# Performance work log

Hardware: AMD Instinct MI355X
Metric: run time of the kernel (lower is better)

The kernel has to match this reference:

```python
import jax, jax.numpy as jnp
import numpy as np

DIM, K, H, D, G = 1024, 4, 8, 128, 4

def rotate_half(x):
    x1, x2 = jnp.split(x, 2, axis=-1)
    return jnp.concatenate([-x2, x1], axis=-1)

def setup_inputs() -> dict:
    key = jax.random.key(0)
    ks = jax.random.split(key, 14)
    s = 0.02
    return {
        "x":  jax.random.normal(ks[0], (1, 2048, DIM), jnp.float32),
        "Wq": jax.random.normal(ks[1], (H * D, DIM), jnp.float32) * s,
        "bq": jnp.zeros((H * D,), jnp.float32),
        "Wk": jax.random.normal(ks[2], (G * D, DIM), jnp.float32) * s,
        "bk": jnp.zeros((G * D,), jnp.float32),
        "Wv": jax.random.normal(ks[3], (G * D, DIM), jnp.float32) * s,
        "bv": jnp.zeros((G * D,), jnp.float32),
        "Wo": jax.random.normal(ks[4], (DIM, H * D), jnp.float32) * s,
        "bo": jnp.zeros((DIM,), jnp.float32),
        "W1": jax.random.normal(ks[5], (DIM * 4, DIM), jnp.float32) * s,
        "b1": jnp.zeros((DIM * 4,), jnp.float32),
        "W2": jax.random.normal(ks[6], (K * DIM, DIM * 4), jnp.float32) * s,
        "b2": jnp.zeros((K * DIM,), jnp.float32),
    }

def reference(x, Wq, bq, Wk, bk, Wv, bv, Wo, bo, W1, b1, W2, b2):
    B, S, _ = x.shape
    q = (x @ Wq.T + bq).reshape(B, S, H, D).transpose(0, 2, 1, 3)  # (B,H,S,D)
    k = (x @ Wk.T + bk).reshape(B, S, G, D).transpose(0, 2, 1, 3)  # (B,G,S,D)
    v = (x @ Wv.T + bv).reshape(B, S, G, D).transpose(0, 2, 1, 3)
    # rotary embedding (same as RotaryEmbedding module)
    inv_freq = 1.0 / (10000.0 ** (jnp.arange(0, D, 2, dtype=jnp.float32) / D))
    t = jnp.arange(S, dtype=jnp.float32)
    freqs = t[:, None] * inv_freq[None, :]
    emb = jnp.concatenate([freqs, freqs], axis=-1)            # (S, D)
    cos = jnp.cos(emb)[None, None, :, :]
    sin = jnp.sin(emb)[None, None, :, :]
    q = q * cos + rotate_half(q) * sin
    k = k * cos + rotate_half(k) * sin
    # every q head attends to every kv group; softmax over j, then sum over g and j
    scores = jnp.einsum('bhid,bgjd->bhgij', q, k) / jnp.sqrt(jnp.float32(D))
    mask = jnp.triu(jnp.ones((S, S), dtype=bool), 1)
    scores = jnp.where(mask[None, None, None, :, :], -jnp.inf, scores)
    w = jax.nn.softmax(scores, axis=-1)
    attn = jnp.einsum('bhgij,bgjd->bhid', w, v)               # (B,H,S,D)
    attn = attn.transpose(0, 2, 1, 3).reshape(B, S, H * D)
    o = attn @ Wo.T + bo
    h1 = jax.nn.silu(o @ W1.T + b1)
    out = (h1 @ W2.T + b2).reshape(B, S, K, DIM)
    return out
```

## Files before the change

kernel.cpp:

```cpp
#include <hip/hip_runtime.h>
#include <hip/hip_bf16.h>

#define SEQ 2048

typedef unsigned short ushort_t;
typedef __attribute__((ext_vector_type(8))) short short8;
typedef __attribute__((ext_vector_type(4))) float f32x4;

__device__ __forceinline__ ushort_t f2bf(float f) {
    __hip_bfloat16 h = __float2bfloat16(f);
    return *reinterpret_cast<ushort_t*>(&h);
}

__device__ __forceinline__ void st(float* p, float v) { *p = v; }
__device__ __forceinline__ void st(ushort_t* p, float v) { *p = f2bf(v); }

__device__ __forceinline__ void gload16(const ushort_t* g, ushort_t* l) {
    __builtin_amdgcn_global_load_lds(
        (const __attribute__((address_space(1))) unsigned int*)g,
        (__attribute__((address_space(3))) unsigned int*)l, 16, 0, 0);
}

__global__ void cvt_bf_kernel(const float* __restrict__ s0, ushort_t* __restrict__ d0, int n0,
                              const float* __restrict__ s1, ushort_t* __restrict__ d1, int n1,
                              const float* __restrict__ s2, ushort_t* __restrict__ d2, int n2,
                              const float* __restrict__ s3, ushort_t* __restrict__ d3, int n3,
                              const float* __restrict__ s4, ushort_t* __restrict__ d4) {
    int u = blockIdx.x * 256 + threadIdx.x;
    const float* s; ushort_t* d;
    if (u < n0) { s = s0; d = d0; }
    else if ((u -= n0) < n1) { s = s1; d = d1; }
    else if ((u -= n1) < n2) { s = s2; d = d2; }
    else if ((u -= n2) < n3) { s = s3; d = d3; }
    else { u -= n3; s = s4; d = d4; }
    float4 a = ((const float4*)s)[u];
    union { ushort_t us[4]; unsigned long long ll; } pk;
    pk.us[0] = f2bf(a.x); pk.us[1] = f2bf(a.y);
    pk.us[2] = f2bf(a.z); pk.us[3] = f2bf(a.w);
    ((unsigned long long*)d)[u] = pk.ll;
}

template <bool SILU, typename TC>
__global__ __launch_bounds__(256) void mfma_gemm_kernel(
    const ushort_t* __restrict__ A, const ushort_t* __restrict__ W,
    const float* __restrict__ bias, TC* __restrict__ C, int M, int N, int Kd) {
    __shared__ __align__(16) ushort_t As[128 * 64];
    __shared__ __align__(16) ushort_t Bs[128 * 64];
    const int tid = threadIdx.x;
    const int w = tid >> 6, lane = tid & 63, l15 = lane & 15, quad = lane >> 4;
    const int m0 = blockIdx.y * 128, n0 = blockIdx.x * 128;
    const int rw = (w >> 1) * 64, cw = (w & 1) * 64;
    const int rA = w * 32 + (lane >> 3);
    const int cch = ((lane & 7) ^ (lane >> 3)) * 8;

    f32x4 acc[4][4];
#pragma unroll
    for (int mt = 0; mt < 4; ++mt)
#pragma unroll
        for (int nt = 0; nt < 4; ++nt) acc[mt][nt] = (f32x4){0.f, 0.f, 0.f, 0.f};

    for (int k0 = 0; k0 < Kd; k0 += 64) {
#pragma unroll
        for (int c = 0; c < 4; ++c) {
            gload16(&A[(size_t)(m0 + rA + c * 8) * Kd + k0 + cch],
                    &As[(w * 4 + c) * 512]);
            gload16(&W[(size_t)(n0 + rA + c * 8) * Kd + k0 + cch],
                    &Bs[(w * 4 + c) * 512]);
        }
        __syncthreads();
#pragma unroll
        for (int kc = 0; kc < 2; ++kc) {
            short8 af[4], bfr[4];
#pragma unroll
            for (int mt = 0; mt < 4; ++mt) {
                int row = rw + mt * 16 + l15;
                int slot = (kc * 4 + quad) ^ (row & 7);
                af[mt] = *(const short8*)&As[row * 64 + slot * 8];
            }
#pragma unroll
            for (int nt = 0; nt < 4; ++nt) {
                int row = cw + nt * 16 + l15;
                int slot = (kc * 4 + quad) ^ (row & 7);
                bfr[nt] = *(const short8*)&Bs[row * 64 + slot * 8];
            }
#pragma unroll
            for (int mt = 0; mt < 4; ++mt)
#pragma unroll
                for (int nt = 0; nt < 4; ++nt)
                    acc[mt][nt] = __builtin_amdgcn_mfma_f32_16x16x32_bf16(
                        af[mt], bfr[nt], acc[mt][nt], 0, 0, 0);
        }
        __syncthreads();
    }
#pragma unroll
    for (int nt = 0; nt < 4; ++nt) {
        int col = n0 + cw + nt * 16 + l15;
        float bb = bias[col];
#pragma unroll
        for (int mt = 0; mt < 4; ++mt)
#pragma unroll
            for (int r = 0; r < 4; ++r) {
                int row = m0 + rw + mt * 16 + quad * 4 + r;
                float v = acc[mt][nt][r] + bb;
                if (SILU) v = v / (1.f + __expf(-v));
                st(&C[(size_t)row * N + col], v);
            }
    }
}

__global__ void rope_bf_kernel(const float* __restrict__ qf, const float* __restrict__ kf,
                               ushort_t* __restrict__ qb, ushort_t* __restrict__ kb) {
    const int s = blockIdx.x;
    const float t = (float)s;
    const float qs = 0.08838834764831845f;
    for (int p = threadIdx.x; p < 768; p += 256) {
        int idx = p & 63;
        float invf = powf(10000.f, -(float)(2 * idx) / 128.f);
        float ang = t * invf;
        float c = cosf(ang), sn = sinf(ang);
        if (p < 512) {
            int h = p >> 6;
            const float* src = qf + (size_t)s * 1024 + h * 128 + idx;
            ushort_t* dst = qb + (size_t)s * 1024 + h * 128 + idx;
            float x1 = src[0], x2 = src[64];
            dst[0] = f2bf((x1 * c - x2 * sn) * qs);
            dst[64] = f2bf((x2 * c + x1 * sn) * qs);
        } else {
            int h = (p - 512) >> 6;
            const float* src = kf + (size_t)s * 512 + h * 128 + idx;
            ushort_t* dst = kb + (size_t)s * 512 + h * 128 + idx;
            float x1 = src[0], x2 = src[64];
            dst[0] = f2bf(x1 * c - x2 * sn);
            dst[64] = f2bf(x2 * c + x1 * sn);
        }
    }
}

__global__ void transpose_v_kernel(const ushort_t* __restrict__ v, ushort_t* __restrict__ vT) {
    __shared__ __align__(16) ushort_t t[64][72];
    const int s0 = blockIdx.x * 64, d0 = blockIdx.y * 64;
    const int tid = threadIdx.x;
#pragma unroll
    for (int it = 0; it < 2; ++it) {
        int u = tid + it * 256;
        int r = u >> 3, c8 = u & 7;
        *(short8*)&t[r][c8 * 8] = *(const short8*)&v[(size_t)(s0 + r) * 512 + d0 + c8 * 8];
    }
    __syncthreads();
#pragma unroll
    for (int it = 0; it < 2; ++it) {
        int u = tid + it * 256;
        int r = u >> 3, c8 = u & 7;
        short8 o;
        ushort_t* op = (ushort_t*)&o;
#pragma unroll
        for (int i = 0; i < 8; ++i) op[i] = t[c8 * 8 + i][r];
        *(short8*)&vT[(size_t)(d0 + r) * 2048 + s0 + c8 * 8] = o;
    }
}

__global__ __launch_bounds__(256, 2) void mfma_attn_kernel(
    const ushort_t* __restrict__ qb, const ushort_t* __restrict__ kb,
    const ushort_t* __restrict__ vT, float* __restrict__ part) {
    const int tid = threadIdx.x;
    const int w = tid >> 6;
    const int lane = tid & 63;
    const int l15 = lane & 15;
    const int quad = lane >> 4;
    const int bx = blockIdx.x;
    const int pr = bx >> 3;
    const int g = (bx >> 1) & 3;
    const int h = (bx & 1) * 4 + w;

    const ushort_t* vtg = vT + (size_t)g * 128 * 2048;

    __shared__ __align__(16) ushort_t Ks[64 * 128];
    __shared__ __align__(16) ushort_t Vs[128 * 64];
    __shared__ __align__(16) ushort_t P_lds[4][16][72];

#pragma unroll 1
    for (int half = 0; half < 2; ++half) {
        const int p = half ? (127 - pr) : pr;
        const int i0 = p << 4;
        const int jmax = p >> 2;
        const int rbase = (p & 3) << 4;

        short8 aq[4];
        {
            const ushort_t* qrow = qb + (size_t)(i0 + l15) * 1024 + h * 128 + quad * 8;
#pragma unroll
            for (int kc = 0; kc < 4; ++kc) aq[kc] = *(const short8*)(qrow + kc * 32);
        }
        f32x4 oacc[8];
#pragma unroll
        for (int nt = 0; nt < 8; ++nt) oacc[nt] = (f32x4){0.f, 0.f, 0.f, 0.f};
        float l_part[4] = {0.f, 0.f, 0.f, 0.f};

        short8 kreg[4], vreg[4];
#pragma unroll
        for (int it = 0; it < 4; ++it) {
            int fl = it * 256 + tid;
            int r = fl >> 4, c8 = fl & 15;
            kreg[it] = *(const short8*)&kb[(size_t)r * 512 + g * 128 + c8 * 8];
        }
#pragma unroll
        for (int it = 0; it < 4; ++it) {
            int fl = it * 256 + tid;
            int r = fl >> 3, c8 = fl & 7;
            vreg[it] = *(const short8*)&vtg[(size_t)r * 2048 + c8 * 8];
        }

        for (int jt = 0; jt <= jmax; ++jt) {
            __syncthreads();
#pragma unroll
            for (int it = 0; it < 4; ++it) {
                int fl = it * 256 + tid;
                int r = fl >> 4, c8 = fl & 15;
                *(short8*)&Ks[r * 128 + ((c8 ^ (r & 7)) * 8)] = kreg[it];
            }
#pragma unroll
            for (int it = 0; it < 4; ++it) {
                int fl = it * 256 + tid;
                int r = fl >> 3, c8 = fl & 7;
                *(short8*)&Vs[r * 64 + ((c8 ^ (r & 7)) * 8)] = vreg[it];
            }
            __syncthreads();
            if (jt < jmax) {
                const int j1 = (jt + 1) << 6;
#pragma unroll
                for (int it = 0; it < 4; ++it) {
                    int fl = it * 256 + tid;
                    int r = fl >> 4, c8 = fl & 15;
                    kreg[it] = *(const short8*)&kb[(size_t)(j1 + r) * 512 + g * 128 + c8 * 8];
                }
#pragma unroll
                for (int it = 0; it < 4; ++it) {
                    int fl = it * 256 + tid;
                    int r = fl >> 3, c8 = fl & 7;
                    vreg[it] = *(const short8*)&vtg[(size_t)r * 2048 + j1 + c8 * 8];
                }
            }
            f32x4 sacc[4];
#pragma unroll
            for (int nt = 0; nt < 4; ++nt) sacc[nt] = (f32x4){0.f, 0.f, 0.f, 0.f};
#pragma unroll
            for (int nt = 0; nt < 4; ++nt) {
                const ushort_t* krow = &Ks[(nt * 16 + l15) * 128];
                const int sw = l15 & 7;
#pragma unroll
                for (int kc = 0; kc < 4; ++kc) {
                    short8 bk = *(const short8*)(krow + (((kc * 4 + quad) ^ sw) * 8));
                    sacc[nt] = __builtin_amdgcn_mfma_f32_16x16x32_bf16(
                        aq[kc], bk, sacc[nt], 0, 0, 0);
                }
            }
            if (jt == jmax) {
#pragma unroll
                for (int nt = 0; nt < 4; ++nt) {
                    int colg = nt * 16 + l15;
#pragma unroll
                    for (int r = 0; r < 4; ++r) {
                        int rowg = rbase + quad * 4 + r;
                        if (colg > rowg) sacc[nt][r] = -1e30f;
                    }
                }
            }
#pragma unroll
            for (int nt = 0; nt < 4; ++nt)
#pragma unroll
                for (int r = 0; r < 4; ++r) {
                    float e = __expf(sacc[nt][r] - 14.f);
                    sacc[nt][r] = e;
                    l_part[r] += e;
                }
#pragma unroll
            for (int nt = 0; nt < 4; ++nt)
#pragma unroll
                for (int r = 0; r < 4; ++r)
                    P_lds[w][quad * 4 + r][nt * 16 + l15] = f2bf(sacc[nt][r]);
            asm volatile("s_waitcnt lgkmcnt(0)" ::: "memory");
            __builtin_amdgcn_sched_barrier(0);
#pragma unroll
            for (int c = 0; c < 2; ++c) {
                short8 ap = *(const short8*)&P_lds[w][l15][c * 32 + quad * 8];
#pragma unroll
                for (int nt = 0; nt < 8; ++nt) {
                    short8 bv = *(const short8*)
                        &Vs[(nt * 16 + l15) * 64 + (((c * 4 + quad) ^ (l15 & 7)) * 8)];
                    oacc[nt] = __builtin_amdgcn_mfma_f32_16x16x32_bf16(
                        ap, bv, oacc[nt], 0, 0, 0);
                }
            }
        }
#pragma unroll
        for (int r = 0; r < 4; ++r) {
            float s = l_part[r];
            s += __shfl_xor(s, 1);
            s += __shfl_xor(s, 2);
            s += __shfl_xor(s, 4);
            s += __shfl_xor(s, 8);
            float inv = 1.f / s;
            int row = i0 + quad * 4 + r;
            float* dst = part + ((size_t)g * SEQ + row) * 1024 + h * 128;
#pragma unroll
            for (int nt = 0; nt < 8; ++nt) dst[nt * 16 + l15] = oacc[nt][r] * inv;
        }
    }
}

__global__ void sum4_bf_kernel(const float* __restrict__ part, ushort_t* __restrict__ attn) {
    int idx = blockIdx.x * 256 + threadIdx.x;
    const float4* p = (const float4*)part;
    float4 a = p[idx];
    float4 b = p[idx + 524288];
    float4 c = p[idx + 2 * 524288];
    float4 d = p[idx + 3 * 524288];
    union { ushort_t u[4]; unsigned long long ll; } pk;
    pk.u[0] = f2bf(a.x + b.x + c.x + d.x);
    pk.u[1] = f2bf(a.y + b.y + c.y + d.y);
    pk.u[2] = f2bf(a.z + b.z + c.z + d.z);
    pk.u[3] = f2bf(a.w + b.w + c.w + d.w);
    *(unsigned long long*)&attn[(size_t)idx * 4] = pk.ll;
}

extern "C" void kernel_launch(void* const* d_in, const int* in_sizes, int n_in,
                              void* d_out, int out_size, void* d_ws, size_t ws_size,
                              hipStream_t stream) {
    const float* x  = (const float*)d_in[0];
    const float* Wq = (const float*)d_in[1];
    const float* bq = (const float*)d_in[2];
    const float* Wk = (const float*)d_in[3];
    const float* bk = (const float*)d_in[4];
    const float* Wv = (const float*)d_in[5];
    const float* bv = (const float*)d_in[6];
    const float* Wo = (const float*)d_in[7];
    const float* bo = (const float*)d_in[8];
    const float* W1 = (const float*)d_in[9];
    const float* b1 = (const float*)d_in[10];
    const float* W2 = (const float*)d_in[11];
    const float* b2 = (const float*)d_in[12];
    float* out = (float*)d_out;

    char* ws = (char*)d_ws;
#define MB(x) ((size_t)(x) << 20)
    float*    part    = (float*)(ws);
    ushort_t* W2_bf   = (ushort_t*)(ws);
    float*    q_f32   = (float*)(ws + MB(32));
    float*    k_f32   = (float*)(ws + MB(40));
    ushort_t* x_bf    = (ushort_t*)(ws + MB(44));
    ushort_t* Wq_bf   = (ushort_t*)(ws + MB(48));
    ushort_t* Wk_bf   = (ushort_t*)(ws + MB(50));
    ushort_t* Wv_bf   = (ushort_t*)(ws + MB(51));
    ushort_t* v_bf    = (ushort_t*)(ws + MB(52));
    ushort_t* vT      = (ushort_t*)(ws + MB(54));
    ushort_t* q_bf    = (ushort_t*)(ws + MB(44));
    ushort_t* k_bf    = (ushort_t*)(ws + MB(48));
    ushort_t* attn_bf = (ushort_t*)(ws + MB(50));
    ushort_t* Wo_bf   = (ushort_t*)(ws + MB(54));
    ushort_t* o_bf    = (ushort_t*)(ws + MB(32));
    ushort_t* h1_bf   = (ushort_t*)(ws + MB(36));
    ushort_t* W1_bf   = (ushort_t*)(ws + MB(56));
#undef MB

    cvt_bf_kernel<<<8192, 256, 0, stream>>>(
        x, x_bf, 524288, Wq, Wq_bf, 262144, Wk, Wk_bf, 131072,
        Wv, Wv_bf, 131072, W1, W1_bf);
    mfma_gemm_kernel<false, float><<<dim3(8, 16), 256, 0, stream>>>(
        x_bf, Wq_bf, bq, q_f32, SEQ, 1024, 1024);
    mfma_gemm_kernel<false, float><<<dim3(4, 16), 256, 0, stream>>>(
        x_bf, Wk_bf, bk, k_f32, SEQ, 512, 1024);
    mfma_gemm_kernel<false, ushort_t><<<dim3(4, 16), 256, 0, stream>>>(
        x_bf, Wv_bf, bv, v_bf, SEQ, 512, 1024);
    transpose_v_kernel<<<dim3(32, 8), 256, 0, stream>>>(v_bf, vT);
    rope_bf_kernel<<<SEQ, 256, 0, stream>>>(q_f32, k_f32, q_bf, k_bf);
    mfma_attn_kernel<<<512, 256, 0, stream>>>(q_bf, k_bf, vT, part);
    sum4_bf_kernel<<<2048, 256, 0, stream>>>(part, attn_bf);
    cvt_bf_kernel<<<17408, 256, 0, stream>>>(
        Wo, Wo_bf, 262144, W2, W2_bf, 4194304, W2, W2_bf, 0,
        W2, W2_bf, 0, W2, W2_bf);
    mfma_gemm_kernel<false, ushort_t><<<dim3(8, 16), 256, 0, stream>>>(
        attn_bf, Wo_bf, bo, o_bf, SEQ, 1024, 1024);
    mfma_gemm_kernel<true, ushort_t><<<dim3(32, 16), 256, 0, stream>>>(
        o_bf, W1_bf, b1, h1_bf, SEQ, 4096, 1024);
    mfma_gemm_kernel<false, float><<<dim3(32, 16), 256, 0, stream>>>(
        h1_bf, W2_bf, b2, out, SEQ, 4096, 4096);
}
```

Baseline: 428.0 us.

## Fuse Q/K/V projections into one GEMM and add XCD-aware block remapping

Places the Wq, Wk and Wv bf16 copies contiguously so a single GEMM produces a fused 2048-wide QKV fp32 output, with a three-way bias select in the epilogue. The V transpose now reads fp32 from the fused buffer and converts to bf16 itself, and RoPE reads Q/K from the fused buffer and computes the inverse frequency with exp2f instead of powf. All GEMMs switch to a 1D grid whose block IDs are remapped round-robin by groups of 8, aiming to keep neighbouring tiles on the same XCD for L2 reuse. This cuts three launches to one and improves occupancy for the small projections, at the cost of writing V as fp32 rather than bf16.

```diff
diff --git a/kernel.cpp b/kernel.cpp
--- a/kernel.cpp
+++ b/kernel.cpp
@@ -43,12 +43,18 @@
 template <bool SILU, typename TC>
 __global__ __launch_bounds__(256) void mfma_gemm_kernel(
     const ushort_t* __restrict__ A, const ushort_t* __restrict__ W,
-    const float* __restrict__ bias, TC* __restrict__ C, int M, int N, int Kd) {
+    const float* __restrict__ bias0, const float* __restrict__ bias1,
+    const float* __restrict__ bias2, int sp1, int sp2,
+    TC* __restrict__ C, int M, int N, int Kd, int NBX) {
     __shared__ __align__(16) ushort_t As[128 * 64];
     __shared__ __align__(16) ushort_t Bs[128 * 64];
     const int tid = threadIdx.x;
     const int w = tid >> 6, lane = tid & 63, l15 = lane & 15, quad = lane >> 4;
-    const int m0 = blockIdx.y * 128, n0 = blockIdx.x * 128;
+    const int nwg = gridDim.x;
+    const int qq = nwg >> 3;
+    const int bid = blockIdx.x;
+    const int sw = (bid & 7) * qq + (bid >> 3);
+    const int m0 = (sw / NBX) * 128, n0 = (sw % NBX) * 128;
     const int rw = (w >> 1) * 64, cw = (w & 1) * 64;
     const int rA = w * 32 + (lane >> 3);
     const int cch = ((lane & 7) ^ (lane >> 3)) * 8;
@@ -95,7 +101,8 @@
 #pragma unroll
     for (int nt = 0; nt < 4; ++nt) {
         int col = n0 + cw + nt * 16 + l15;
-        float bb = bias[col];
+        float bb = col < sp1 ? bias0[col]
+                 : (col < sp2 ? bias1[col - sp1] : bias2[col - sp2]);
 #pragma unroll
         for (int mt = 0; mt < 4; ++mt)
 #pragma unroll
@@ -108,26 +115,26 @@
     }
 }
 
-__global__ void rope_bf_kernel(const float* __restrict__ qf, const float* __restrict__ kf,
+__global__ void rope_bf_kernel(const float* __restrict__ qkv,
                                ushort_t* __restrict__ qb, ushort_t* __restrict__ kb) {
     const int s = blockIdx.x;
     const float t = (float)s;
     const float qs = 0.08838834764831845f;
     for (int p = threadIdx.x; p < 768; p += 256) {
         int idx = p & 63;
-        float invf = powf(10000.f, -(float)(2 * idx) / 128.f);
+        float invf = exp2f(-(float)idx * 0.20762050593f);
         float ang = t * invf;
         float c = cosf(ang), sn = sinf(ang);
         if (p < 512) {
             int h = p >> 6;
-            const float* src = qf + (size_t)s * 1024 + h * 128 + idx;
+            const float* src = qkv + (size_t)s * 2048 + h * 128 + idx;
             ushort_t* dst = qb + (size_t)s * 1024 + h * 128 + idx;
             float x1 = src[0], x2 = src[64];
             dst[0] = f2bf((x1 * c - x2 * sn) * qs);
             dst[64] = f2bf((x2 * c + x1 * sn) * qs);
         } else {
             int h = (p - 512) >> 6;
-            const float* src = kf + (size_t)s * 512 + h * 128 + idx;
+            const float* src = qkv + (size_t)s * 2048 + 1024 + h * 128 + idx;
             ushort_t* dst = kb + (size_t)s * 512 + h * 128 + idx;
             float x1 = src[0], x2 = src[64];
             dst[0] = f2bf(x1 * c - x2 * sn);
@@ -136,15 +143,19 @@
     }
 }
 
-__global__ void transpose_v_kernel(const ushort_t* __restrict__ v, ushort_t* __restrict__ vT) {
+__global__ void transpose_v_kernel(const float* __restrict__ qkv, ushort_t* __restrict__ vT) {
     __shared__ __align__(16) ushort_t t[64][72];
     const int s0 = blockIdx.x * 64, d0 = blockIdx.y * 64;
     const int tid = threadIdx.x;
 #pragma unroll
-    for (int it = 0; it < 2; ++it) {
+    for (int it = 0; it < 4; ++it) {
         int u = tid + it * 256;
-        int r = u >> 3, c8 = u & 7;
-        *(short8*)&t[r][c8 * 8] = *(const short8*)&v[(size_t)(s0 + r) * 512 + d0 + c8 * 8];
+        int r = u >> 4, c4 = u & 15;
+        float4 a = *(const float4*)&qkv[(size_t)(s0 + r) * 2048 + 1536 + d0 + c4 * 4];
+        union { ushort_t us[4]; unsigned long long ll; } pk;
+        pk.us[0] = f2bf(a.x); pk.us[1] = f2bf(a.y);
+        pk.us[2] = f2bf(a.z); pk.us[3] = f2bf(a.w);
+        *(unsigned long long*)&t[r][c4 * 4] = pk.ll;
     }
     __syncthreads();
 #pragma unroll
@@ -345,43 +356,38 @@
 #define MB(x) ((size_t)(x) << 20)
     float*    part    = (float*)(ws);
     ushort_t* W2_bf   = (ushort_t*)(ws);
-    float*    q_f32   = (float*)(ws + MB(32));
-    float*    k_f32   = (float*)(ws + MB(40));
-    ushort_t* x_bf    = (ushort_t*)(ws + MB(44));
-    ushort_t* Wq_bf   = (ushort_t*)(ws + MB(48));
-    ushort_t* Wk_bf   = (ushort_t*)(ws + MB(50));
-    ushort_t* Wv_bf   = (ushort_t*)(ws + MB(51));
-    ushort_t* v_bf    = (ushort_t*)(ws + MB(52));
+    float*    qkv_f32 = (float*)(ws + MB(32));
+    ushort_t* o_bf    = (ushort_t*)(ws + MB(32));
+    ushort_t* attn_bf = (ushort_t*)(ws + MB(36));
+    ushort_t* h1_bf   = (ushort_t*)(ws + MB(40));
+    ushort_t* x_bf    = (ushort_t*)(ws + MB(48));
+    ushort_t* q_bf    = (ushort_t*)(ws + MB(48));
+    ushort_t* Wqkv_bf = (ushort_t*)(ws + MB(52));
+    ushort_t* Wq_bf   = (ushort_t*)(ws + MB(52));
+    ushort_t* Wk_bf   = (ushort_t*)(ws + MB(54));
+    ushort_t* Wv_bf   = (ushort_t*)(ws + MB(55));
+    ushort_t* k_bf    = (ushort_t*)(ws + MB(52));
     ushort_t* vT      = (ushort_t*)(ws + MB(54));
-    ushort_t* q_bf    = (ushort_t*)(ws + MB(44));
-    ushort_t* k_bf    = (ushort_t*)(ws + MB(48));
-    ushort_t* attn_bf = (ushort_t*)(ws + MB(50));
     ushort_t* Wo_bf   = (ushort_t*)(ws + MB(54));
-    ushort_t* o_bf    = (ushort_t*)(ws + MB(32));
-    ushort_t* h1_bf   = (ushort_t*)(ws + MB(36));
     ushort_t* W1_bf   = (ushort_t*)(ws + MB(56));
 #undef MB
 
     cvt_bf_kernel<<<8192, 256, 0, stream>>>(
         x, x_bf, 524288, Wq, Wq_bf, 262144, Wk, Wk_bf, 131072,
         Wv, Wv_bf, 131072, W1, W1_bf);
-    mfma_gemm_kernel<false, float><<<dim3(8, 16), 256, 0, stream>>>(
-        x_bf, Wq_bf, bq, q_f32, SEQ, 1024, 1024);
-    mfma_gemm_kernel<false, float><<<dim3(4, 16), 256, 0, stream>>>(
-        x_bf, Wk_bf, bk, k_f32, SEQ, 512, 1024);
-    mfma_gemm_kernel<false, ushort_t><<<dim3(4, 16), 256, 0, stream>>>(
-        x_bf, Wv_bf, bv, v_bf, SEQ, 512, 1024);
-    transpose_v_kernel<<<dim3(32, 8), 256, 0, stream>>>(v_bf, vT);
-    rope_bf_kernel<<<SEQ, 256, 0, stream>>>(q_f32, k_f32, q_bf, k_bf);
+    mfma_gemm_kernel<false, float><<<256, 256, 0, stream>>>(
+        x_bf, Wqkv_bf, bq, bk, bv, 1024, 1536, qkv_f32, SEQ, 2048, 1024, 16);
+    transpose_v_kernel<<<dim3(32, 8), 256, 0, stream>>>(qkv_f32, vT);
+    rope_bf_kernel<<<SEQ, 256, 0, stream>>>(qkv_f32, q_bf, k_bf);
     mfma_attn_kernel<<<512, 256, 0, stream>>>(q_bf, k_bf, vT, part);
     sum4_bf_kernel<<<2048, 256, 0, stream>>>(part, attn_bf);
     cvt_bf_kernel<<<17408, 256, 0, stream>>>(
         Wo, Wo_bf, 262144, W2, W2_bf, 4194304, W2, W2_bf, 0,
         W2, W2_bf, 0, W2, W2_bf);
-    mfma_gemm_kernel<false, ushort_t><<<dim3(8, 16), 256, 0, stream>>>(
-        attn_bf, Wo_bf, bo, o_bf, SEQ, 1024, 1024);
-    mfma_gemm_kernel<true, ushort_t><<<dim3(32, 16), 256, 0, stream>>>(
-        o_bf, W1_bf, b1, h1_bf, SEQ, 4096, 1024);
-    mfma_gemm_kernel<false, float><<<dim3(32, 16), 256, 0, stream>>>(
-        h1_bf, W2_bf, b2, out, SEQ, 4096, 4096);
-}
+    mfma_gemm_kernel<false, ushort_t><<<128, 256, 0, stream>>>(
+        attn_bf, Wo_bf, bo, bo, bo, 1024, 1024, o_bf, SEQ, 1024, 1024, 8);
+    mfma_gemm_kernel<true, ushort_t><<<512, 256, 0, stream>>>(
+        o_bf, W1_bf, b1, b1, b1, 4096, 4096, h1_bf, SEQ, 4096, 1024, 32);
+    mfma_gemm_kernel<false, float><<<512, 256, 0, stream>>>(
+        h1_bf, W2_bf, b2, b2, b2, 4096, 4096, out, SEQ, 4096, 4096, 32);
+}
```

Result: faster. 393.8 us (-8.0%).
